# Performance work log

Measured on AMD Instinct MI355X. Metric: run time of the kernel, lower is better.

## Reference

```python
import jax, jax.numpy as jnp
import numpy as np

B, S, D, C = 2, 4096, 768, 8192
SCALE = 1.0
LN_EPS = 1e-5


def setup_inputs() -> dict:
    key = jax.random.key(0)
    ks = jax.random.split(key, 8)
    std = 0.03
    return {
        "x": jax.random.normal(ks[0], (B, S, D), dtype=jnp.float32),
        "attention_masks": jax.random.randint(ks[1], (B, S), 0, 2).astype(jnp.int32),
        "Wk": jax.random.normal(ks[2], (D, D), dtype=jnp.float32) * std,
        "Wv": jax.random.normal(ks[3], (D, D), dtype=jnp.float32) * std,
        "bv": jnp.zeros((D,), dtype=jnp.float32),
        "Q": jax.random.normal(ks[4], (C, D), dtype=jnp.float32) * std,  # label_representations
        "ln_gamma": jnp.ones((D,), dtype=jnp.float32),
        "ln_beta": jnp.zeros((D,), dtype=jnp.float32),
        "w_out": jax.random.normal(ks[5], (D,), dtype=jnp.float32) * std,  # output_linear.weight [1, D]
        "b_out": jnp.zeros((), dtype=jnp.float32),  # output_linear.bias [1]
    }


def reference(x, attention_masks, Wk, Wv, bv, Q, ln_gamma, ln_beta, w_out, b_out):
    # K, V projections (torch Linear: x @ W.T + b)
    K = jnp.einsum("bsd,ed->bse", x, Wk)
    V = jnp.einsum("bsd,ed->bse", x, Wv) + bv
    # label-query cross-attention scores: [B, C, S]
    scores = jnp.einsum("cd,bsd->bcs", Q, K)
    # additive mask: -inf where attention_masks == 0 (intended semantics of pad/repeat/masked_fill)
    scores = jnp.where(attention_masks[:, None, :] == 0, -jnp.inf, scores)
    attn = jax.nn.softmax(scores / SCALE, axis=2)  # [B, C, S]
    y = jnp.einsum("bcs,bsd->bcd", attn, V)  # [B, C, D]
    # LayerNorm over last dim
    mu = jnp.mean(y, axis=-1, keepdims=True)
    var = jnp.mean((y - mu) ** 2, axis=-1, keepdims=True)
    y = (y - mu) * jax.lax.rsqrt(var + LN_EPS) * ln_gamma + ln_beta
    # elementwise weight-mul-sum output head: [B, C]
    return jnp.einsum("bcd,d->bc", y, w_out) + b_out
```

## Files before the change

kernel.cpp:

```cpp
#include <hip/hip_runtime.h>
#include <hip/hip_bf16.h>
#include <hip/hip_fp16.h>

typedef _Float16 f16x8 __attribute__((ext_vector_type(8)));
typedef _Float16 f16x4 __attribute__((ext_vector_type(4)));
typedef float f32x4 __attribute__((ext_vector_type(4)));

#define AS1 __attribute__((address_space(1)))
#define AS3 __attribute__((address_space(3)))
#define MFMA16(a, b, c) __builtin_amdgcn_mfma_f32_16x16x32_f16(a, b, c, 0, 0, 0)

#define LDP 2304

__global__ __launch_bounds__(256) void maskscan(const int* __restrict__ am,
                                                int* __restrict__ idx,
                                                int* __restrict__ meta) {
  const int b = blockIdx.x, t = threadIdx.x;
  const int* m = am + (size_t)b * 4096;
  int* ix = idx + (size_t)b * 4096;
  __shared__ int cnt[256];
  __shared__ int pre[257];
  int loc[16], c = 0;
#pragma unroll
  for (int j = 0; j < 16; ++j) {
    loc[j] = m[t * 16 + j];
    c += (loc[j] != 0);
  }
  cnt[t] = c;
  __syncthreads();
  if (t == 0) {
    pre[0] = 0;
    for (int i = 0; i < 256; ++i) pre[i + 1] = pre[i] + cnt[i];
  }
  __syncthreads();
  int p = pre[t];
#pragma unroll
  for (int j = 0; j < 16; ++j)
    if (loc[j]) ix[p++] = t * 16 + j;
  const int valid = pre[256];
  int nsp = ((valid + 255) >> 8) << 8;
  if (nsp < 512) nsp = 512;
  for (int j = valid + t; j < nsp; j += 256) ix[j] = -1;
  if (t == 0) { meta[2 * b] = valid; meta[2 * b + 1] = nsp; }
}

__global__ __launch_bounds__(192) void gather_cvt(const float* __restrict__ x,
                                                  const int* __restrict__ idx,
                                                  const int* __restrict__ meta,
                                                  unsigned short* __restrict__ xc) {
  const int b = blockIdx.y, row = blockIdx.x, t = threadIdx.x;
  if (row >= meta[2 * b + 1]) return;
  const int src = idx[(size_t)b * 4096 + row];
  unsigned short* dst = xc + ((size_t)b * 4096 + row) * 768 + t * 4;
  f16x4 h;
  if (src < 0) {
    h[0] = h[1] = h[2] = h[3] = (_Float16)0.0f;
  } else {
    float4 v = *(const float4*)(x + ((size_t)b * 4096 + src) * 768 + t * 4);
    h[0] = (_Float16)v.x; h[1] = (_Float16)v.y; h[2] = (_Float16)v.z; h[3] = (_Float16)v.w;
  }
  *(f16x4*)dst = h;
}

__global__ __launch_bounds__(256) void cvt_f32_f16(const float* __restrict__ in,
                                                   unsigned short* __restrict__ out,
                                                   int n8) {
  int i = blockIdx.x * 256 + threadIdx.x;
  if (i >= n8) return;
  const float4* p = (const float4*)in + 2 * (size_t)i;
  float4 a = p[0], b = p[1];
  f16x8 h;
  h[0] = (_Float16)a.x; h[1] = (_Float16)a.y; h[2] = (_Float16)a.z; h[3] = (_Float16)a.w;
  h[4] = (_Float16)b.x; h[5] = (_Float16)b.y; h[6] = (_Float16)b.z; h[7] = (_Float16)b.w;
  *(f16x8*)(out + (size_t)i * 8) = h;
}

template <int OMODE, bool RBIAS, int EXITD>
__global__ __launch_bounds__(256) void gemm_nt(const unsigned short* __restrict__ A, int lda,
                                               const unsigned short* __restrict__ B, int ldb,
                                               void* __restrict__ Cout, int ldc,
                                               const float* __restrict__ bias,
                                               const int* __restrict__ meta,
                                               int N, int K) {
  const int nbn = N >> 7;
  const int bm = blockIdx.x / nbn, bn = blockIdx.x % nbn;
  if constexpr (EXITD == 1) {
    if (((bm & 31) << 7) >= meta[2 * (bm >> 5) + 1]) return;
  } else if constexpr (EXITD == 2) {
    if (((bn & 31) << 7) >= meta[2 * (bn >> 5) + 1]) return;
  }
  __shared__ __attribute__((aligned(16))) unsigned short As[128 * 64];
  __shared__ __attribute__((aligned(16))) unsigned short Bs[128 * 64];
  const int tid = threadIdx.x;
  const int w = tid >> 6, l = tid & 63;
  const int wr = w >> 1, wc = w & 1;
  const int lr = l & 15, lg = l >> 4;

  const unsigned short* Ab = A + (size_t)bm * 128 * lda;
  const unsigned short* Bb = B + (size_t)bn * 128 * ldb;

  f32x4 acc[4][4] = {};

  auto ldfrag = [&](const unsigned short* base, int row, int kk) {
    int off = row * 128 + kk * 64 + lg * 16;
    off ^= (row & 7) << 4;
    return *(const f16x8*)((const unsigned char*)base + off);
  };

  for (int kt = 0; kt < K; kt += 64) {
#pragma unroll
    for (int i = 0; i < 4; ++i) {
      const int c = i * 256 + w * 64 + l;
      const int row = c >> 3, col = (((c & 7) ^ (row & 7)) << 3);
      __builtin_amdgcn_global_load_lds((const AS1 void*)(Ab + (size_t)row * lda + kt + col),
                                       (AS3 void*)(As + (i * 256 + w * 64) * 8), 16, 0, 0);
    }
#pragma unroll
    for (int i = 0; i < 4; ++i) {
      const int c = i * 256 + w * 64 + l;
      const int row = c >> 3, col = (((c & 7) ^ (row & 7)) << 3);
      __builtin_amdgcn_global_load_lds((const AS1 void*)(Bb + (size_t)row * ldb + kt + col),
                                       (AS3 void*)(Bs + (i * 256 + w * 64) * 8), 16, 0, 0);
    }
    __syncthreads();
#pragma unroll
    for (int kk = 0; kk < 2; ++kk) {
      f16x8 af[4], bf[4];
#pragma unroll
      for (int mi = 0; mi < 4; ++mi) af[mi] = ldfrag(As, wr * 64 + mi * 16 + lr, kk);
#pragma unroll
      for (int ni = 0; ni < 4; ++ni) bf[ni] = ldfrag(Bs, wc * 64 + ni * 16 + lr, kk);
#pragma unroll
      for (int mi = 0; mi < 4; ++mi)
#pragma unroll
        for (int ni = 0; ni < 4; ++ni)
          acc[mi][ni] = MFMA16(af[mi], bf[ni], acc[mi][ni]);
    }
    __syncthreads();
  }

#pragma unroll
  for (int mi = 0; mi < 4; ++mi) {
#pragma unroll
    for (int r = 0; r < 4; ++r) {
      const int row = bm * 128 + wr * 64 + mi * 16 + lg * 4 + r;
      const float badd = RBIAS ? bias[row] : 0.0f;
#pragma unroll
      for (int ni = 0; ni < 4; ++ni) {
        const int col = bn * 128 + wc * 64 + ni * 16 + lr;
        float v = acc[mi][ni][r] + badd;
        if constexpr (OMODE == 0)
          ((unsigned short*)Cout)[(size_t)row * ldc + col] =
              __builtin_bit_cast(unsigned short, (_Float16)v);
        else
          ((float*)Cout)[(size_t)row * ldc + col] = v;
      }
    }
  }
}

#define VM8 asm volatile("s_waitcnt vmcnt(8)" ::: "memory")
#define VM4 asm volatile("s_waitcnt vmcnt(4)" ::: "memory")
#define VM0 asm volatile("s_waitcnt vmcnt(0)" ::: "memory")
#define VMNONE ((void)0)
#define BARRIER asm volatile("s_barrier" ::: "memory")

#define PH(kk, mh, VMW)                                                        \
  {                                                                            \
    f16x8 a0 = ldA8(4 * (mh) + 0, (kk));                                       \
    f16x8 a1 = ldA8(4 * (mh) + 1, (kk));                                       \
    f16x8 a2 = ldA8(4 * (mh) + 2, (kk));                                       \
    f16x8 a3 = ldA8(4 * (mh) + 3, (kk));                                       \
    f16x8 b0 = ldB8(0, (kk));                                                  \
    f16x8 b1 = ldB8(1, (kk));                                                  \
    f16x8 b2 = ldB8(2, (kk));                                                  \
    f16x8 b3 = ldB8(3, (kk));                                                  \
    if (u < NT4) stage(u);                                                     \
    ++u;                                                                       \
    BARRIER;                                                                   \
    __builtin_amdgcn_s_setprio(1);                                             \
    acc[4 * (mh) + 0][0] = MFMA16(a0, b0, acc[4 * (mh) + 0][0]);               \
    acc[4 * (mh) + 0][1] = MFMA16(a0, b1, acc[4 * (mh) + 0][1]);               \
    acc[4 * (mh) + 0][2] = MFMA16(a0, b2, acc[4 * (mh) + 0][2]);               \
    acc[4 * (mh) + 0][3] = MFMA16(a0, b3, acc[4 * (mh) + 0][3]);               \
    acc[4 * (mh) + 1][0] = MFMA16(a1, b0, acc[4 * (mh) + 1][0]);               \
    acc[4 * (mh) + 1][1] = MFMA16(a1, b1, acc[4 * (mh) + 1][1]);               \
    acc[4 * (mh) + 1][2] = MFMA16(a1, b2, acc[4 * (mh) + 1][2]);               \
    acc[4 * (mh) + 1][3] = MFMA16(a1, b3, acc[4 * (mh) + 1][3]);               \
    acc[4 * (mh) + 2][0] = MFMA16(a2, b0, acc[4 * (mh) + 2][0]);               \
    acc[4 * (mh) + 2][1] = MFMA16(a2, b1, acc[4 * (mh) + 2][1]);               \
    acc[4 * (mh) + 2][2] = MFMA16(a2, b2, acc[4 * (mh) + 2][2]);               \
    acc[4 * (mh) + 2][3] = MFMA16(a2, b3, acc[4 * (mh) + 2][3]);               \
    acc[4 * (mh) + 3][0] = MFMA16(a3, b0, acc[4 * (mh) + 3][0]);               \
    acc[4 * (mh) + 3][1] = MFMA16(a3, b1, acc[4 * (mh) + 3][1]);               \
    acc[4 * (mh) + 3][2] = MFMA16(a3, b2, acc[4 * (mh) + 3][2]);               \
    acc[4 * (mh) + 3][3] = MFMA16(a3, b3, acc[4 * (mh) + 3][3]);               \
    __builtin_amdgcn_s_setprio(0);                                             \
    VMW;                                                                       \
    BARRIER;                                                                   \
  }

template <int EPI>
__global__ __launch_bounds__(512, 2) void gemm256(
    const unsigned short* __restrict__ A, int lda, size_t sAz,
    const unsigned short* __restrict__ B, int ldb, size_t sBz,
    unsigned short* __restrict__ Cout, int ldc, size_t sCz, size_t sCk,
    const int* __restrict__ meta, int NTfix) {
  __shared__ __attribute__((aligned(16))) unsigned char lds[131072];
  const int tid = threadIdx.x;
  const int wv = tid >> 6, l = tid & 63;
  const int wm = wv >> 2, wn = wv & 3;
  const int lr = l & 15, lg = l >> 4;

  const int bid = blockIdx.x;

  const unsigned short* Ab = nullptr;
  const unsigned short* Bb = nullptr;
  int bufOff = 0;

  auto stage = [&](int uu) {
    const int tau = uu >> 2, r = uu & 3;
    const int regionOff = ((tau & 1) << 16) | ((r & 1) << 15) | ((r >> 1) << 14);
    const unsigned short* base = (r & 1) ? Bb : Ab;
    const int ld = (r & 1) ? ldb : lda;
    const int kcol0 = tau * 64 + ((r >> 1) << 5);
#pragma unroll
    for (int j = 0; j < 2; ++j) {
      const int row = wv * 32 + j * 16 + (l >> 2);
      const int col = kcol0 + ((((l & 3) ^ ((row >> 1) & 3))) << 3);
      __builtin_amdgcn_global_load_lds(
          (const AS1 void*)(base + (size_t)row * ld + col),
          (AS3 void*)(lds + regionOff + wv * 2048 + j * 1024), 16, 0, 0);
    }
  };
  auto ldA8 = [&](int mf, int kk) {
    const int row = wm * 128 + mf * 16 + lr;
    int off = (row << 6) + (lg << 4);
    off ^= ((row >> 1) & 3) << 4;
    return *(const f16x8*)(lds + bufOff + (kk << 14) + off);
  };
  auto ldB8 = [&](int nf, int kk) {
    const int row = wn * 64 + nf * 16 + lr;
    int off = (row << 6) + (lg << 4);
    off ^= ((row >> 1) & 3) << 4;
    return *(const f16x8*)(lds + bufOff + 32768 + (kk << 14) + off);
  };

  constexpr int NPASS = (EPI == 2) ? 2 : 1;

  for (int pass = 0; pass < NPASS; ++pass) {
    int z, bm, bn, NT, koff, ks = 0;
    if constexpr (EPI == 2) {
      if (pass == 0) {
        z = bid >> 8;
        const int rem = bid & 255;
        bm = rem & 31;
        bn = rem >> 5;
        if (bn * 256 >= meta[2 * z + 1]) continue;
      } else {
        const int tn0 = max(0, (meta[1] >> 8) - 8);
        const int tn1 = max(0, (meta[3] >> 8) - 8);
        if (bid >= 32 * (tn0 + tn1)) break;
        int t = bid;
        if (t < 32 * tn0) { z = 0; }
        else { t -= 32 * tn0; z = 1; }
        bm = t & 31;
        bn = 8 + (t >> 5);
      }
      NT = NTfix;
      koff = 0;
    } else {
      z = bid / 192;
      const int r = bid - z * 192;
      ks = r / 96;
      const int q = r - ks * 96;
      bm = q & 31;
      bn = q >> 5;
      const int nsp = meta[2 * z + 1];
      NT = nsp >> 7;
      koff = ks * (nsp >> 1);
    }
    const int valid = meta[2 * z];

    Ab = A + (size_t)z * sAz + koff + (size_t)bm * 256 * lda;
    Bb = B + (size_t)z * sBz + koff + (size_t)bn * 256 * ldb;

    const int NT4 = NT * 4;
    f32x4 acc[8][4] = {};

    for (int i = 0; i < 6; ++i) stage(i);
    int u = 6;
    VM8;
    BARRIER;

    for (int t = 0; t + 2 < NT; ++t) {
      bufOff = (t & 1) << 16;
      PH(0, 0, VMNONE);
      PH(0, 1, VM8);
      PH(1, 0, VMNONE);
      PH(1, 1, VM8);
    }
    bufOff = ((NT - 2) & 1) << 16;
    PH(0, 0, VMNONE);
    PH(0, 1, VM8);
    PH(1, 0, VMNONE);
    PH(1, 1, VM4);
    bufOff = ((NT - 1) & 1) << 16;
    PH(0, 0, VMNONE);
    PH(0, 1, VM0);
    PH(1, 0, VMNONE);
    PH(1, 1, VMNONE);

    const size_t crow0 = (size_t)bm * 256 + wm * 128;
    const int ccol0 = bn * 256 + wn * 64;
    unsigned short* Cz = Cout + (size_t)z * sCz + (size_t)ks * sCk;
#pragma unroll
    for (int mf = 0; mf < 8; ++mf) {
#pragma unroll
      for (int rr = 0; rr < 4; ++rr) {
        const size_t rb = (crow0 + mf * 16 + lg * 4 + rr) * (size_t)ldc;
#pragma unroll
        for (int nf = 0; nf < 4; ++nf) {
          const int col = ccol0 + nf * 16 + lr;
          float v = acc[mf][nf][rr];
          if constexpr (EPI == 2) v = (col < valid) ? __expf(v) : 0.0f;
          Cz[rb + col] = __builtin_bit_cast(unsigned short, (_Float16)v);
        }
      }
    }
  }
}

__device__ inline float block_sum(float v, float* sh, int t) {
#pragma unroll
  for (int o = 32; o; o >>= 1) v += __shfl_xor(v, o);
  __syncthreads();
  if ((t & 63) == 0) sh[t >> 6] = v;
  __syncthreads();
  return sh[0] + sh[1] + sh[2] + sh[3];
}

__global__ __launch_bounds__(256) void ln_head(const unsigned short* __restrict__ yp,
                                               size_t zoff, size_t koff,
                                               const float* __restrict__ gam,
                                               const float* __restrict__ bet,
                                               const float* __restrict__ wo,
                                               const float* __restrict__ bo,
                                               float* __restrict__ out) {
  const int z = blockIdx.y;
  const size_t rbase = (size_t)z * zoff + (size_t)blockIdx.x * 768;
  const _Float16* y0 = (const _Float16*)yp + rbase;
  const _Float16* y1 = y0 + koff;
  const int t = threadIdx.x;
  float a0 = (float)y0[t] + (float)y1[t];
  float a1 = (float)y0[t + 256] + (float)y1[t + 256];
  float a2 = (float)y0[t + 512] + (float)y1[t + 512];
  __shared__ float sh[4];
  float s = block_sum(a0 + a1 + a2, sh, t);
  float mu = s * (1.0f / 768.0f);
  float d0 = a0 - mu, d1 = a1 - mu, d2 = a2 - mu;
  float q = block_sum(d0 * d0 + d1 * d1 + d2 * d2, sh, t);
  float rs = rsqrtf(q * (1.0f / 768.0f) + 1e-5f);
  float o = (d0 * rs * gam[t] + bet[t]) * wo[t] +
            (d1 * rs * gam[t + 256] + bet[t + 256]) * wo[t + 256] +
            (d2 * rs * gam[t + 512] + bet[t + 512]) * wo[t + 512];
  o = block_sum(o, sh, t);
  if (t == 0) out[(size_t)z * 8192 + blockIdx.x] = o + bo[0];
}

extern "C" void kernel_launch(void* const* d_in, const int* in_sizes, int n_in,
                              void* d_out, int out_size, void* d_ws, size_t ws_size,
                              hipStream_t stream) {
  const float* x  = (const float*)d_in[0];
  const int*   am = (const int*)d_in[1];
  const float* Wk = (const float*)d_in[2];
  const float* Wv = (const float*)d_in[3];
  const float* bv = (const float*)d_in[4];
  const float* Q  = (const float*)d_in[5];
  const float* gam = (const float*)d_in[6];
  const float* bet = (const float*)d_in[7];
  const float* wo  = (const float*)d_in[8];
  const float* bo  = (const float*)d_in[9];
  float* out = (float*)d_out;

  const int S = 4096, D = 768, C = 8192;
  const size_t nX = (size_t)2 * S * D;
  const size_t nW = (size_t)D * D;
  const size_t nQ = (size_t)C * D;
  const size_t nPc = (size_t)C * LDP;
  const size_t nY = (size_t)C * D;

  unsigned short* xc  = (unsigned short*)d_ws;
  unsigned short* Wkb = xc + nX;
  unsigned short* Wvb = Wkb + nW;
  unsigned short* Qb  = Wvb + nW;
  unsigned short* Kb  = Qb + nQ;
  unsigned short* Vt  = Kb + nX;
  unsigned short* P   = Vt + nX;
  unsigned short* yp  = P + 2 * nPc;
  int* idx  = (int*)(yp + 4 * nY);
  int* meta = idx + 2 * 4096;

  maskscan<<<2, 256, 0, stream>>>(am, idx, meta);
  gather_cvt<<<dim3(4096, 2), 192, 0, stream>>>(x, idx, meta, xc);

  cvt_f32_f16<<<(int)(nW / 8 / 256), 256, 0, stream>>>(Wk, Wkb, (int)(nW / 8));
  cvt_f32_f16<<<(int)(nW / 8 / 256), 256, 0, stream>>>(Wv, Wvb, (int)(nW / 8));
  cvt_f32_f16<<<(int)(nQ / 8 / 256), 256, 0, stream>>>(Q, Qb, (int)(nQ / 8));

  gemm_nt<0, false, 1><<<(8192 / 128) * (768 / 128), 256, 0, stream>>>(
      xc, D, Wkb, D, Kb, D, nullptr, meta, 768, D);
  gemm_nt<0, true, 2><<<(768 / 128) * (8192 / 128), 256, 0, stream>>>(
      Wvb, D, xc, D, Vt, 2 * S, bv, meta, 2 * S, D);

  gemm256<2><<<dim3(512, 1), 512, 0, stream>>>(
      Qb, D, 0, Kb, D, (size_t)S * D, P, LDP, nPc, 0, meta, 12);

  gemm256<0><<<dim3(384, 1), 512, 0, stream>>>(
      P, LDP, nPc, Vt, 2 * S, (size_t)S, yp, D, 2 * nY, nY, meta, 0);

  ln_head<<<dim3(C, 2), 256, 0, stream>>>(yp, 2 * nY, nY, gam, bet, wo, bo, out);
}
```

Measured before the change: 234.3 us.

## Software-pipeline LDS fragment reads with MFMAs and halve barriers in gemm256 main loop

Replaces the phase macro, which read all A/B fragments and then ran 16 MFMAs between two barriers, with a rolled loop that double-buffers register fragments. Each group's LDS reads now overlap the MFMAs of the previous group, and there is one barrier per phase instead of two. LDS address offsets are precomputed once per thread, and the vmcnt waits are changed to match. This hides LDS latency behind compute but uses more registers under launch_bounds(512,2). The tighter barrier and waitcnt choreography also risks races on the staged buffers.

```diff
diff --git a/kernel.cpp b/kernel.cpp
--- a/kernel.cpp
+++ b/kernel.cpp
@@ -9,6 +9,7 @@
 #define AS1 __attribute__((address_space(1)))
 #define AS3 __attribute__((address_space(3)))
 #define MFMA16(a, b, c) __builtin_amdgcn_mfma_f32_16x16x32_f16(a, b, c, 0, 0, 0)
+#define BARRIER asm volatile("s_barrier" ::: "memory")
 
 #define LDP 2304
 
@@ -159,47 +160,6 @@
   }
 }
 
-#define VM8 asm volatile("s_waitcnt vmcnt(8)" ::: "memory")
-#define VM4 asm volatile("s_waitcnt vmcnt(4)" ::: "memory")
-#define VM0 asm volatile("s_waitcnt vmcnt(0)" ::: "memory")
-#define VMNONE ((void)0)
-#define BARRIER asm volatile("s_barrier" ::: "memory")
-
-#define PH(kk, mh, VMW)                                                        \
-  {                                                                            \
-    f16x8 a0 = ldA8(4 * (mh) + 0, (kk));                                       \
-    f16x8 a1 = ldA8(4 * (mh) + 1, (kk));                                       \
-    f16x8 a2 = ldA8(4 * (mh) + 2, (kk));                                       \
-    f16x8 a3 = ldA8(4 * (mh) + 3, (kk));                                       \
-    f16x8 b0 = ldB8(0, (kk));                                                  \
-    f16x8 b1 = ldB8(1, (kk));                                                  \
-    f16x8 b2 = ldB8(2, (kk));                                                  \
-    f16x8 b3 = ldB8(3, (kk));                                                  \
-    if (u < NT4) stage(u);                                                     \
-    ++u;                                                                       \
-    BARRIER;                                                                   \
-    __builtin_amdgcn_s_setprio(1);                                             \
-    acc[4 * (mh) + 0][0] = MFMA16(a0, b0, acc[4 * (mh) + 0][0]);               \
-    acc[4 * (mh) + 0][1] = MFMA16(a0, b1, acc[4 * (mh) + 0][1]);               \
-    acc[4 * (mh) + 0][2] = MFMA16(a0, b2, acc[4 * (mh) + 0][2]);               \
-    acc[4 * (mh) + 0][3] = MFMA16(a0, b3, acc[4 * (mh) + 0][3]);               \
-    acc[4 * (mh) + 1][0] = MFMA16(a1, b0, acc[4 * (mh) + 1][0]);               \
-    acc[4 * (mh) + 1][1] = MFMA16(a1, b1, acc[4 * (mh) + 1][1]);               \
-    acc[4 * (mh) + 1][2] = MFMA16(a1, b2, acc[4 * (mh) + 1][2]);               \
-    acc[4 * (mh) + 1][3] = MFMA16(a1, b3, acc[4 * (mh) + 1][3]);               \
-    acc[4 * (mh) + 2][0] = MFMA16(a2, b0, acc[4 * (mh) + 2][0]);               \
-    acc[4 * (mh) + 2][1] = MFMA16(a2, b1, acc[4 * (mh) + 2][1]);               \
-    acc[4 * (mh) + 2][2] = MFMA16(a2, b2, acc[4 * (mh) + 2][2]);               \
-    acc[4 * (mh) + 2][3] = MFMA16(a2, b3, acc[4 * (mh) + 2][3]);               \
-    acc[4 * (mh) + 3][0] = MFMA16(a3, b0, acc[4 * (mh) + 3][0]);               \
-    acc[4 * (mh) + 3][1] = MFMA16(a3, b1, acc[4 * (mh) + 3][1]);               \
-    acc[4 * (mh) + 3][2] = MFMA16(a3, b2, acc[4 * (mh) + 3][2]);               \
-    acc[4 * (mh) + 3][3] = MFMA16(a3, b3, acc[4 * (mh) + 3][3]);               \
-    __builtin_amdgcn_s_setprio(0);                                             \
-    VMW;                                                                       \
-    BARRIER;                                                                   \
-  }
-
 template <int EPI>
 __global__ __launch_bounds__(512, 2) void gemm256(
     const unsigned short* __restrict__ A, int lda, size_t sAz,
@@ -211,12 +171,14 @@
   const int wv = tid >> 6, l = tid & 63;
   const int wm = wv >> 2, wn = wv & 3;
   const int lr = l & 15, lg = l >> 4;
-
   const int bid = blockIdx.x;
+
+  const int xr = ((lr >> 1) & 3) << 4;
+  const int aoff = ((wm * 128 + lr) << 6) + ((lg << 4) ^ xr);
+  const int boff = ((wn * 64 + lr) << 6) + ((lg << 4) ^ xr);
 
   const unsigned short* Ab = nullptr;
   const unsigned short* Bb = nullptr;
-  int bufOff = 0;
 
   auto stage = [&](int uu) {
     const int tau = uu >> 2, r = uu & 3;
@@ -232,18 +194,6 @@
           (const AS1 void*)(base + (size_t)row * ld + col),
           (AS3 void*)(lds + regionOff + wv * 2048 + j * 1024), 16, 0, 0);
     }
-  };
-  auto ldA8 = [&](int mf, int kk) {
-    const int row = wm * 128 + mf * 16 + lr;
-    int off = (row << 6) + (lg << 4);
-    off ^= ((row >> 1) & 3) << 4;
-    return *(const f16x8*)(lds + bufOff + (kk << 14) + off);
-  };
-  auto ldB8 = [&](int nf, int kk) {
-    const int row = wn * 64 + nf * 16 + lr;
-    int off = (row << 6) + (lg << 4);
-    off ^= ((row >> 1) & 3) << 4;
-    return *(const f16x8*)(lds + bufOff + 32768 + (kk << 14) + off);
   };
 
   constexpr int NPASS = (EPI == 2) ? 2 : 1;
@@ -287,29 +237,69 @@
 
     const int NT4 = NT * 4;
     f32x4 acc[8][4] = {};
+    f16x8 Ac[4], An[4], Bc[4], B2[4];
+
+    auto rdA4 = [&](f16x8* d, int mh, int kk, int bo) {
+#pragma unroll
+      for (int i = 0; i < 4; ++i)
+        d[i] = *(const f16x8*)(lds + bo + (kk << 14) + aoff + (4 * mh + i) * 1024);
+    };
+    auto rdB4 = [&](f16x8* d, int kk, int bo) {
+#pragma unroll
+      for (int i = 0; i < 4; ++i)
+        d[i] = *(const f16x8*)(lds + 32768 + bo + (kk << 14) + boff + i * 1024);
+    };
+    auto mm16 = [&](const f16x8* Aq, const f16x8* Bq, int mh) {
+#pragma unroll
+      for (int i = 0; i < 4; ++i)
+#pragma unroll
+        for (int j = 0; j < 4; ++j)
+          acc[4 * mh + i][j] = MFMA16(Aq[i], Bq[j], acc[4 * mh + i][j]);
+    };
 
     for (int i = 0; i < 6; ++i) stage(i);
     int u = 6;
-    VM8;
+    asm volatile("s_waitcnt vmcnt(4)" ::: "memory");
     BARRIER;
 
-    for (int t = 0; t + 2 < NT; ++t) {
-      bufOff = (t & 1) << 16;
-      PH(0, 0, VMNONE);
-      PH(0, 1, VM8);
-      PH(1, 0, VMNONE);
-      PH(1, 1, VM8);
-    }
-    bufOff = ((NT - 2) & 1) << 16;
-    PH(0, 0, VMNONE);
-    PH(0, 1, VM8);
-    PH(1, 0, VMNONE);
-    PH(1, 1, VM4);
-    bufOff = ((NT - 1) & 1) << 16;
-    PH(0, 0, VMNONE);
-    PH(0, 1, VM0);
-    PH(1, 0, VMNONE);
-    PH(1, 1, VMNONE);
+    for (int t = 0; t < NT; ++t) {
+      const int bo = (t & 1) << 16;
+      rdB4(Bc, 0, bo);
+      rdA4(Ac, 0, 0, bo);
+      if (u < NT4) stage(u);
+      ++u;
+      __builtin_amdgcn_s_setprio(1);
+      rdA4(An, 1, 0, bo);
+      mm16(Ac, Bc, 0);
+      __builtin_amdgcn_s_setprio(0);
+      BARRIER;
+      if (u < NT4) stage(u);
+      ++u;
+      __builtin_amdgcn_s_setprio(1);
+      rdB4(B2, 1, bo);
+      rdA4(Ac, 0, 1, bo);
+      mm16(An, Bc, 1);
+      __builtin_amdgcn_s_setprio(0);
+      BARRIER;
+      if (u < NT4) stage(u);
+      ++u;
+      __builtin_amdgcn_s_setprio(1);
+      rdA4(An, 1, 1, bo);
+      mm16(Ac, B2, 0);
+      __builtin_amdgcn_s_setprio(0);
+      BARRIER;
+      if (u < NT4) stage(u);
+      ++u;
+      __builtin_amdgcn_s_setprio(1);
+      mm16(An, B2, 1);
+      __builtin_amdgcn_s_setprio(0);
+      if (t + 2 < NT) {
+        asm volatile("s_waitcnt vmcnt(4)" ::: "memory");
+      } else if (t + 2 == NT) {
+        asm volatile("s_waitcnt vmcnt(0)" ::: "memory");
+      }
+      BARRIER;
+    }
 
     const size_t crow0 = (size_t)bm * 256 + wm * 128;
     const int ccol0 = bn * 256 + wn * 64;
```

Result: faster. 224.7 us (-4.1%).
